# Kernel optimization log

Hardware: AMD Instinct MI355X
Metric: run time of the kernel (lower is better)

The kernel has to match this reference:

```python
import jax, jax.numpy as jnp
import numpy as np

DIM = 768
NUM_HEADS = 12
HEAD_DIM = DIM // NUM_HEADS
SCALE = HEAD_DIM ** -0.5
B, N = 8, 1024


def setup_inputs() -> dict:
    key = jax.random.key(0)
    k1, k2, k3, k4 = jax.random.split(key, 4)
    s = 1.0 / np.sqrt(DIM)
    return {
        "x": jax.random.normal(k1, (B, N, DIM), dtype=jnp.float32),
        "w_qkv": jax.random.normal(k2, (DIM, 3 * DIM), dtype=jnp.float32) * s,  # qkv_bias=False
        "w_proj": jax.random.normal(k3, (DIM, DIM), dtype=jnp.float32) * s,
        "b_proj": jax.random.normal(k4, (DIM,), dtype=jnp.float32) * 0.01,
    }


def reference(x, w_qkv, w_proj, b_proj):
    Bb, Nn, C = x.shape
    qkv = x @ w_qkv  # [B, N, 3C]
    qkv = qkv.reshape(Bb, Nn, 3, NUM_HEADS, HEAD_DIM)
    q = qkv[:, :, 0].transpose(0, 2, 1, 3)  # [B, H, N, d]
    k = qkv[:, :, 1].transpose(0, 2, 1, 3)
    v = qkv[:, :, 2].transpose(0, 2, 1, 3)
    attn = jnp.einsum("bhqd,bhkd->bhqk", q, k) * SCALE
    attn = jax.nn.softmax(attn, axis=-1)  # dropout p=0 -> identity
    out = jnp.einsum("bhqk,bhkd->bhqd", attn, v)
    out = out.transpose(0, 2, 1, 3).reshape(Bb, Nn, C)
    return out @ w_proj + b_proj
```

## Files before the change

### kernel.cpp

```cpp
#include <hip/hip_runtime.h>
#include <stdint.h>

typedef __attribute__((ext_vector_type(8))) __bf16 bf16x8;
typedef __attribute__((ext_vector_type(8))) unsigned short u16x8;
typedef __attribute__((ext_vector_type(4))) unsigned short u16x4;
typedef __attribute__((ext_vector_type(4))) short s16x4;
typedef __attribute__((ext_vector_type(4))) float f32x4;

typedef unsigned int u32_as1 __attribute__((address_space(1)));
typedef unsigned int u32_as3 __attribute__((address_space(3)));

__device__ __forceinline__ unsigned short f2bf(float f) {
  unsigned int u = __float_as_uint(f);
  u += 0x7fffu + ((u >> 16) & 1u);
  return (unsigned short)(u >> 16);
}

__device__ __forceinline__ bf16x8 ld_frag(const unsigned short* p) {
  return __builtin_bit_cast(bf16x8, *(const u16x8*)p);
}

__device__ __forceinline__ f32x4 mfma16(s16x4 a, s16x4 b, f32x4 c) {
#if __has_builtin(__builtin_amdgcn_mfma_f32_16x16x16bf16_1k)
  return __builtin_amdgcn_mfma_f32_16x16x16bf16_1k(a, b, c, 0, 0, 0);
#elif __has_builtin(__builtin_amdgcn_mfma_f32_16x16x16_bf16_1k)
  return __builtin_amdgcn_mfma_f32_16x16x16_bf16_1k(a, b, c, 0, 0, 0);
#else
  asm volatile("v_mfma_f32_16x16x16_bf16 %0, %1, %2, %0"
               : "+v"(c) : "v"(a), "v"(b));
  return c;
#endif
}

__device__ __forceinline__ float fast_exp2(float x) {
#if __has_builtin(__builtin_amdgcn_exp2f)
  return __builtin_amdgcn_exp2f(x);
#else
  return exp2f(x);
#endif
}

__device__ __forceinline__ void async16(const void* g, void* l) {
  const u32_as1* gp = (const u32_as1*)(uintptr_t)g;
  u32_as3* lp = (u32_as3*)(uintptr_t)l;
  __builtin_amdgcn_global_load_lds(gp, lp, 16, 0, 0);
}

template <int N> __device__ __forceinline__ void wait_vmcnt() {
  if constexpr (N == 0) asm volatile("s_waitcnt vmcnt(0)" ::: "memory");
  else if constexpr (N == 3) asm volatile("s_waitcnt vmcnt(3)" ::: "memory");
  else if constexpr (N == 4) asm volatile("s_waitcnt vmcnt(4)" ::: "memory");
}
__device__ __forceinline__ void barrier_raw() {
  asm volatile("s_barrier" ::: "memory");
}

__global__ __launch_bounds__(256) void prep_kernel(
    const float* __restrict__ x, const float* __restrict__ w_qkv,
    const float* __restrict__ w_proj, u16x4* __restrict__ x_bf,
    unsigned short* __restrict__ wqkvT, unsigned short* __restrict__ wprojT) {
  const int bid = blockIdx.x;
  const int t = threadIdx.x;
  if (bid < 6144) {
    const int i = bid * 256 + t;
    float4 v = ((const float4*)x)[i];
    u16x4 o;
    o[0] = f2bf(v.x); o[1] = f2bf(v.y); o[2] = f2bf(v.z); o[3] = f2bf(v.w);
    x_bf[i] = o;
    return;
  }
  __shared__ float tile[32][33];
  const float* w; unsigned short* wt; int N, bx, by;
  if (bid < 6144 + 1728) { const int r = bid - 6144; w = w_qkv; wt = wqkvT; N = 2304; bx = r % 72; by = r / 72; }
  else                   { const int r = bid - 7872; w = w_proj; wt = wprojT; N = 768; bx = r % 24; by = r / 24; }
  const int n0 = bx * 32, k0 = by * 32;
  const int tx = t & 31, ty = t >> 5;
#pragma unroll
  for (int r = 0; r < 4; r++)
    tile[ty + r * 8][tx] = w[(k0 + ty + r * 8) * N + n0 + tx];
  __syncthreads();
#pragma unroll
  for (int r = 0; r < 4; r++)
    wt[(n0 + ty + r * 8) * 768 + k0 + tx] = f2bf(tile[tx][ty + r * 8]);
}

template <int EPI, int NT, int NBLK>
__global__ __launch_bounds__(256, 4) void gemm_bt(
    const unsigned short* __restrict__ A, const unsigned short* __restrict__ Bt,
    unsigned short* __restrict__ qb, unsigned short* __restrict__ kb,
    unsigned short* __restrict__ vtb, float* __restrict__ outp,
    const float* __restrict__ bias) {
  constexpr int STAGE = 4096 + NT * 2048;
  constexpr int NK = 24;
  constexpr int NL = NT + 2;
  __shared__ unsigned short smem[3 * STAGE];

  const int t = threadIdx.x;
  const int lane = t & 63, w = t >> 6;
  const int quad = lane >> 4, l15 = lane & 15;

  const int bid = blockIdx.x;
  const int xcd = bid & 7, slot = bid >> 3;
  const int m0 = (xcd * 8 + slot / NBLK) * 128;
  const int n0 = (slot % NBLK) * (NT * 64);
  const int wm = (w & 1) * 64, wn = (w >> 1) * (NT * 32);

  f32x4 acc[4][NT * 2];
  const f32x4 fzero = {0.f, 0.f, 0.f, 0.f};
#pragma unroll
  for (int i = 0; i < 4; i++)
#pragma unroll
    for (int j = 0; j < NT * 2; j++) acc[i][j] = fzero;

  const int srow = w * 16 + (lane >> 2);
  const int scol = (((lane & 3) - (srow >> 1)) & 3) * 8;
  const unsigned short* Ag = A + (m0 + srow) * 768 + scol;
  const unsigned short* Bg = Bt + (n0 + srow) * 768 + scol;
  const int ldso = w * 512 + lane * 8;

  auto fill = [&](int ktile, int buf) {
    const int kcol = ktile * 32;
    unsigned short* As = smem + buf * STAGE;
    unsigned short* Bs = As + 4096;
    async16(Ag + kcol, As + ldso);
    async16(Ag + 64 * 768 + kcol, As + ldso + 2048);
#pragma unroll
    for (int f = 0; f < NT; f++)
      async16(Bg + f * 64 * 768 + kcol, Bs + ldso + f * 2048);
  };

  fill(0, 0);
  fill(1, 1);
  int cur = 0;
  for (int k = 0; k < NK; ++k) {
    if (k < NK - 1) wait_vmcnt<NL>(); else wait_vmcnt<0>();
    barrier_raw();
    if (k + 2 < NK) {
      int tgt = cur + 2; if (tgt >= 3) tgt -= 3;
      fill(k + 2, tgt);
    }
    const unsigned short* As = smem + cur * STAGE;
    const unsigned short* Bs = As + 4096;

    bf16x8 af[4], bfr[NT * 2];
#pragma unroll
    for (int i = 0; i < 4; i++) {
      const int row = wm + i * 16 + l15;
      af[i] = ld_frag(As + row * 32 + (((quad + (row >> 1)) & 3) << 3));
    }
#pragma unroll
    for (int j = 0; j < NT * 2; j++) {
      const int row = wn + j * 16 + l15;
      bfr[j] = ld_frag(Bs + row * 32 + (((quad + (row >> 1)) & 3) << 3));
    }
#pragma unroll
    for (int i = 0; i < 4; i++)
#pragma unroll
      for (int j = 0; j < NT * 2; j++)
        acc[i][j] = __builtin_amdgcn_mfma_f32_16x16x32_bf16(af[i], bfr[j], acc[i][j], 0, 0, 0);

    cur += 1; if (cur == 3) cur = 0;
  }

#pragma unroll
  for (int i = 0; i < 4; i++) {
    const int gmb = m0 + wm + i * 16 + quad * 4;
#pragma unroll
    for (int j = 0; j < NT * 2; j++) {
      const int gc = n0 + wn + j * 16 + l15;
#pragma unroll
      for (int r = 0; r < 4; r++) {
        const int gm = gmb + r;
        float v = acc[i][j][r];
        if (EPI == 0) {
          const int b = gm >> 10, tok = gm & 1023;
          const int which = (gc >= 1536) ? 2 : (gc >= 768 ? 1 : 0);
          const int rem = gc - which * 768;
          const int h = rem >> 6, d = rem & 63;
          const int bh = b * 12 + h;
          const unsigned short bv = f2bf(v);
          if (which == 0)      qb[(bh << 16) + (tok << 6) + d] = bv;
          else if (which == 1) kb[(bh << 16) + (tok << 6) + d] = bv;
          else                 vtb[(bh << 16) + (d << 10) + tok] = bv;
        } else {
          outp[gm * 768 + gc] = v + bias[gc];
        }
      }
    }
  }
}

#define SWZC(row, c) (((row) << 6) + ((((c) + (row)) & 7) << 3))
#define C2 0.1803368801111244f

__global__ __launch_bounds__(256, 3) void attn_kernel(
    const unsigned short* __restrict__ qb, const unsigned short* __restrict__ kb,
    const unsigned short* __restrict__ vtb, unsigned short* __restrict__ aout) {
  __shared__ unsigned short smem[3 * 8192];

  const int t = threadIdx.x;
  const int lane = t & 63, w = t >> 6;
  const int quad = lane >> 4, l15 = lane & 15;
  const int bh = blockIdx.x;
  const int b = bh / 12, h = bh - b * 12;
  const int q0 = blockIdx.y * 128;
  const int base = bh << 16;

  bf16x8 qf[2][2];
#pragma unroll
  for (int qt = 0; qt < 2; qt++)
#pragma unroll
    for (int s = 0; s < 2; s++)
      qf[qt][s] = ld_frag(qb + base + ((q0 + w * 32 + qt * 16 + l15) << 6) +
                          s * 32 + quad * 8);

  f32x4 oacc[4][2];
  const f32x4 fzero = {0.f, 0.f, 0.f, 0.f};
#pragma unroll
  for (int dt = 0; dt < 4; dt++) { oacc[dt][0] = fzero; oacc[dt][1] = fzero; }
  float lsum0 = 0.f, lsum1 = 0.f;

  const int srow = t >> 3, schk = t & 7;
  const int c0 = ((schk - srow) & 7) * 8;
  const int c1 = ((schk - (srow + 32)) & 7) * 8;

  auto fillkv = [&](int tile, int buf) {
    const int kv0 = tile * 64;
    unsigned short* Ks = smem + buf * 8192;
    unsigned short* Vts = Ks + 4096;
    async16(kb + base + ((kv0 + srow) << 6) + c0, Ks + t * 8);
    async16(kb + base + ((kv0 + srow + 32) << 6) + c1, Ks + 2048 + t * 8);
    async16(vtb + base + (srow << 10) + kv0 + c0, Vts + t * 8);
    async16(vtb + base + ((srow + 32) << 10) + kv0 + c1, Vts + 2048 + t * 8);
  };

  fillkv(0, 0);
  fillkv(1, 1);
  int cur = 0;
  for (int it = 0; it < 16; ++it) {
    if (it < 15) wait_vmcnt<4>(); else wait_vmcnt<0>();
    barrier_raw();
    if (it + 2 < 16) {
      int tgt = cur + 2; if (tgt >= 3) tgt -= 3;
      fillkv(it + 2, tgt);
    }
    const unsigned short* Ks = smem + cur * 8192;
    const unsigned short* Vts = Ks + 4096;

    f32x4 st[4][2];
#pragma unroll
    for (int tc = 0; tc < 4; tc++) { st[tc][0] = fzero; st[tc][1] = fzero; }
#pragma unroll
    for (int s = 0; s < 2; s++) {
#pragma unroll
      for (int tc = 0; tc < 4; tc++) {
        const bf16x8 kf = ld_frag(Ks + SWZC(tc * 16 + l15, s * 4 + quad));
        st[tc][0] = __builtin_amdgcn_mfma_f32_16x16x32_bf16(kf, qf[0][s], st[tc][0], 0, 0, 0);
        st[tc][1] = __builtin_amdgcn_mfma_f32_16x16x32_bf16(kf, qf[1][s], st[tc][1], 0, 0, 0);
      }
    }

    s16x4 pf[4][2];
#pragma unroll
    for (int tc = 0; tc < 4; tc++) {
#pragma unroll
      for (int qt = 0; qt < 2; qt++) {
        const float p0 = fast_exp2(st[tc][qt][0] * C2);
        const float p1 = fast_exp2(st[tc][qt][1] * C2);
        const float p2 = fast_exp2(st[tc][qt][2] * C2);
        const float p3 = fast_exp2(st[tc][qt][3] * C2);
        const float ps = (p0 + p1) + (p2 + p3);
        if (qt == 0) lsum0 += ps; else lsum1 += ps;
        s16x4 pk;
        pk[0] = (short)f2bf(p0); pk[1] = (short)f2bf(p1);
        pk[2] = (short)f2bf(p2); pk[3] = (short)f2bf(p3);
        pf[tc][qt] = pk;
      }
    }

#pragma unroll
    for (int tc = 0; tc < 4; tc++) {
#pragma unroll
      for (int dt = 0; dt < 4; dt++) {
        const int row = dt * 16 + l15;
        const int addr = (row << 6) + ((((tc * 2 + (quad >> 1)) + row) & 7) << 3) +
                         ((quad & 1) << 2);
        const s16x4 vf = *(const s16x4*)(Vts + addr);
        oacc[dt][0] = mfma16(vf, pf[tc][0], oacc[dt][0]);
        oacc[dt][1] = mfma16(vf, pf[tc][1], oacc[dt][1]);
      }
    }

    cur += 1; if (cur == 3) cur = 0;
  }

  lsum0 += __shfl_xor(lsum0, 16); lsum0 += __shfl_xor(lsum0, 32);
  lsum1 += __shfl_xor(lsum1, 16); lsum1 += __shfl_xor(lsum1, 32);
  const float inv0 = 1.f / lsum0, inv1 = 1.f / lsum1;

  __syncthreads();
  unsigned short* Ot = smem;
#pragma unroll
  for (int dt = 0; dt < 4; dt++) {
#pragma unroll
    for (int qt = 0; qt < 2; qt++) {
      const float inv = qt == 0 ? inv0 : inv1;
      const int qrow = (w * 32 + qt * 16 + l15) * 72 + dt * 16 + quad * 4;
#pragma unroll
      for (int r = 0; r < 4; r++)
        Ot[qrow + r] = f2bf(oacc[dt][qt][r] * inv);
    }
  }
  __syncthreads();
#pragma unroll
  for (int it = 0; it < 4; it++) {
    const int q = it * 32 + (t >> 3);
    const int d0 = (t & 7) * 8;
    const u16x8 v = *(const u16x8*)(Ot + q * 72 + d0);
    *(u16x8*)(aout + (b * 1024 + q0 + q) * 768 + h * 64 + d0) = v;
  }
}

extern "C" void kernel_launch(void* const* d_in, const int* in_sizes, int n_in,
                              void* d_out, int out_size, void* d_ws, size_t ws_size,
                              hipStream_t stream) {
  (void)in_sizes; (void)n_in; (void)out_size; (void)ws_size;
  const float* x = (const float*)d_in[0];
  const float* w_qkv = (const float*)d_in[1];
  const float* w_proj = (const float*)d_in[2];
  const float* b_proj = (const float*)d_in[3];
  float* out = (float*)d_out;

  char* ws = (char*)d_ws;
  unsigned short* x_bf   = (unsigned short*)(ws);
  unsigned short* wqkvT  = (unsigned short*)(ws + 12582912);
  unsigned short* wprojT = (unsigned short*)(ws + 16121856);
  unsigned short* qb     = (unsigned short*)(ws + 17301504);
  unsigned short* kb     = (unsigned short*)(ws + 29884416);
  unsigned short* vtb    = (unsigned short*)(ws + 42467328);
  unsigned short* aout   = x_bf;

  prep_kernel<<<8448, 256, 0, stream>>>(x, w_qkv, w_proj, (u16x4*)x_bf, wqkvT, wprojT);
  gemm_bt<0, 2, 18><<<1152, 256, 0, stream>>>(x_bf, wqkvT, qb, kb, vtb, nullptr, nullptr);
  attn_kernel<<<dim3(96, 8), 256, 0, stream>>>(qb, kb, vtb, aout);
  gemm_bt<1, 1, 12><<<768, 256, 0, stream>>>(aout, wprojT, nullptr, nullptr, nullptr, out, b_proj);
}
```

Before: 202.4 us.

## Replace async global-to-LDS triple buffering with register-staged double buffering in GEMM

The GEMM kernels stop using direct global_load_lds into a three-stage LDS ring. They now load tiles into registers two steps ahead and write them to a two-stage LDS buffer after each compute step, with an lgkmcnt wait plus barrier. Minimum waves per EU for the QKV GEMM drops from 4 to 3, which leaves room for the extra staging registers. This cuts LDS footprint and changes the load/compute overlap, at the cost of more VGPR pressure, possibly lower occupancy, and extra ds_write instructions.

New measurement: 199.6 us. About the same (-1.4%).

```diff
diff --git a/kernel.cpp b/kernel.cpp
--- a/kernel.cpp
+++ b/kernel.cpp
@@ -46,13 +46,12 @@
   __builtin_amdgcn_global_load_lds(gp, lp, 16, 0, 0);
 }
 
+__device__ __forceinline__ void lds_barrier() {
+  asm volatile("s_waitcnt lgkmcnt(0)\ns_barrier" ::: "memory");
+}
 template <int N> __device__ __forceinline__ void wait_vmcnt() {
   if constexpr (N == 0) asm volatile("s_waitcnt vmcnt(0)" ::: "memory");
-  else if constexpr (N == 3) asm volatile("s_waitcnt vmcnt(3)" ::: "memory");
   else if constexpr (N == 4) asm volatile("s_waitcnt vmcnt(4)" ::: "memory");
-}
-__device__ __forceinline__ void barrier_raw() {
-  asm volatile("s_barrier" ::: "memory");
 }
 
 __global__ __launch_bounds__(256) void prep_kernel(
@@ -84,16 +83,16 @@
     wt[(n0 + ty + r * 8) * 768 + k0 + tx] = f2bf(tile[tx][ty + r * 8]);
 }
 
-template <int EPI, int NT, int NBLK>
-__global__ __launch_bounds__(256, 4) void gemm_bt(
+template <int EPI, int NT, int NBLK, int MINW>
+__global__ __launch_bounds__(256, MINW) void gemm_bt(
     const unsigned short* __restrict__ A, const unsigned short* __restrict__ Bt,
     unsigned short* __restrict__ qb, unsigned short* __restrict__ kb,
     unsigned short* __restrict__ vtb, float* __restrict__ outp,
     const float* __restrict__ bias) {
   constexpr int STAGE = 4096 + NT * 2048;
   constexpr int NK = 24;
-  constexpr int NL = NT + 2;
-  __shared__ unsigned short smem[3 * STAGE];
+  constexpr int NLD = 2 + NT;
+  __shared__ unsigned short smem[2 * STAGE];
 
   const int t = threadIdx.x;
   const int lane = t & 63, w = t >> 6;
@@ -118,28 +117,33 @@
   const unsigned short* Bg = Bt + (n0 + srow) * 768 + scol;
   const int ldso = w * 512 + lane * 8;
 
-  auto fill = [&](int ktile, int buf) {
-    const int kcol = ktile * 32;
-    unsigned short* As = smem + buf * STAGE;
-    unsigned short* Bs = As + 4096;
-    async16(Ag + kcol, As + ldso);
-    async16(Ag + 64 * 768 + kcol, As + ldso + 2048);
+  u16x8 rb[2][NLD];
+
+  auto g2r = [&](int k, u16x8* r) {
+    r[0] = *(const u16x8*)(Ag + k * 32);
+    r[1] = *(const u16x8*)(Ag + 64 * 768 + k * 32);
 #pragma unroll
     for (int f = 0; f < NT; f++)
-      async16(Bg + f * 64 * 768 + kcol, Bs + ldso + f * 2048);
+      r[2 + f] = *(const u16x8*)(Bg + f * 64 * 768 + k * 32);
   };
-
-  fill(0, 0);
-  fill(1, 1);
-  int cur = 0;
+  auto r2l = [&](int k, const u16x8* r) {
+    unsigned short* As = smem + (k & 1) * STAGE;
+    *(u16x8*)(As + ldso) = r[0];
+    *(u16x8*)(As + ldso + 2048) = r[1];
+#pragma unroll
+    for (int f = 0; f < NT; f++)
+      *(u16x8*)(As + 4096 + ldso + f * 2048) = r[2 + f];
+  };
+
+  g2r(0, rb[0]);
+  g2r(1, rb[1]);
+  r2l(0, rb[0]);
+  lds_barrier();
+  g2r(2, rb[0]);
+
+#pragma unroll
   for (int k = 0; k < NK; ++k) {
-    if (k < NK - 1) wait_vmcnt<NL>(); else wait_vmcnt<0>();
-    barrier_raw();
-    if (k + 2 < NK) {
-      int tgt = cur + 2; if (tgt >= 3) tgt -= 3;
-      fill(k + 2, tgt);
-    }
-    const unsigned short* As = smem + cur * STAGE;
+    const unsigned short* As = smem + (k & 1) * STAGE;
     const unsigned short* Bs = As + 4096;
 
     bf16x8 af[4], bfr[NT * 2];
@@ -159,7 +163,9 @@
       for (int j = 0; j < NT * 2; j++)
         acc[i][j] = __builtin_amdgcn_mfma_f32_16x16x32_bf16(af[i], bfr[j], acc[i][j], 0, 0, 0);
 
-    cur += 1; if (cur == 3) cur = 0;
+    if (k + 1 < NK) r2l(k + 1, rb[(k + 1) & 1]);
+    if (k + 3 < NK) g2r(k + 3, rb[(k + 1) & 1]);
+    if (k + 1 < NK) lds_barrier();
   }
 
 #pragma unroll
@@ -239,7 +245,7 @@
   int cur = 0;
   for (int it = 0; it < 16; ++it) {
     if (it < 15) wait_vmcnt<4>(); else wait_vmcnt<0>();
-    barrier_raw();
+    asm volatile("s_barrier" ::: "memory");
     if (it + 2 < 16) {
       int tgt = cur + 2; if (tgt >= 3) tgt -= 3;
       fillkv(it + 2, tgt);
@@ -341,7 +347,7 @@
   unsigned short* aout   = x_bf;
 
   prep_kernel<<<8448, 256, 0, stream>>>(x, w_qkv, w_proj, (u16x4*)x_bf, wqkvT, wprojT);
-  gemm_bt<0, 2, 18><<<1152, 256, 0, stream>>>(x_bf, wqkvT, qb, kb, vtb, nullptr, nullptr);
+  gemm_bt<0, 2, 18, 3><<<1152, 256, 0, stream>>>(x_bf, wqkvT, qb, kb, vtb, nullptr, nullptr);
   attn_kernel<<<dim3(96, 8), 256, 0, stream>>>(qb, kb, vtb, aout);
-  gemm_bt<1, 1, 12><<<768, 256, 0, stream>>>(aout, wprojT, nullptr, nullptr, nullptr, out, b_proj);
-}
+  gemm_bt<1, 1, 12, 4><<<768, 256, 0, stream>>>(aout, wprojT, nullptr, nullptr, nullptr, out, b_proj);
+}
```

## Replace LDS-staged GEMM with direct global-to-register double-buffered loads

Applied to the files above, without the earlier changes.

The QKV and projection GEMMs no longer stage A and B tiles through LDS with async global_load_lds and a three-buffer ring plus barriers. Each wave now loads its MFMA fragments straight from global memory into registers, double-buffered one k-step ahead with the loop fully unrolled. Launch-bounds occupancy hints are lowered to 2 and 3 waves per SIMD. This removes the LDS round trip and block-wide barriers, but gives up reuse of shared tiles between waves, so global and L2 traffic rises and register pressure grows.

New measurement: 320.7 us. 1.58x slower.

```diff
diff --git a/kernel.cpp b/kernel.cpp
--- a/kernel.cpp
+++ b/kernel.cpp
@@ -18,6 +18,9 @@
 
 __device__ __forceinline__ bf16x8 ld_frag(const unsigned short* p) {
   return __builtin_bit_cast(bf16x8, *(const u16x8*)p);
+}
+__device__ __forceinline__ bf16x8 as_bf(u16x8 v) {
+  return __builtin_bit_cast(bf16x8, v);
 }
 
 __device__ __forceinline__ f32x4 mfma16(s16x4 a, s16x4 b, f32x4 c) {
@@ -48,11 +51,7 @@
 
 template <int N> __device__ __forceinline__ void wait_vmcnt() {
   if constexpr (N == 0) asm volatile("s_waitcnt vmcnt(0)" ::: "memory");
-  else if constexpr (N == 3) asm volatile("s_waitcnt vmcnt(3)" ::: "memory");
   else if constexpr (N == 4) asm volatile("s_waitcnt vmcnt(4)" ::: "memory");
-}
-__device__ __forceinline__ void barrier_raw() {
-  asm volatile("s_barrier" ::: "memory");
 }
 
 __global__ __launch_bounds__(256) void prep_kernel(
@@ -84,17 +83,13 @@
     wt[(n0 + ty + r * 8) * 768 + k0 + tx] = f2bf(tile[tx][ty + r * 8]);
 }
 
-template <int EPI, int NT, int NBLK>
-__global__ __launch_bounds__(256, 4) void gemm_bt(
+template <int EPI, int NT, int NBLK, int MINW>
+__global__ __launch_bounds__(256, MINW) void gemm_direct(
     const unsigned short* __restrict__ A, const unsigned short* __restrict__ Bt,
     unsigned short* __restrict__ qb, unsigned short* __restrict__ kb,
     unsigned short* __restrict__ vtb, float* __restrict__ outp,
     const float* __restrict__ bias) {
-  constexpr int STAGE = 4096 + NT * 2048;
   constexpr int NK = 24;
-  constexpr int NL = NT + 2;
-  __shared__ unsigned short smem[3 * STAGE];
-
   const int t = threadIdx.x;
   const int lane = t & 63, w = t >> 6;
   const int quad = lane >> 4, l15 = lane & 15;
@@ -105,6 +100,9 @@
   const int n0 = (slot % NBLK) * (NT * 64);
   const int wm = (w & 1) * 64, wn = (w >> 1) * (NT * 32);
 
+  const unsigned short* Ap = A + (m0 + wm + l15) * 768 + quad * 8;
+  const unsigned short* Bp = Bt + (n0 + wn + l15) * 768 + quad * 8;
+
   f32x4 acc[4][NT * 2];
   const f32x4 fzero = {0.f, 0.f, 0.f, 0.f};
 #pragma unroll
@@ -112,54 +110,27 @@
 #pragma unroll
     for (int j = 0; j < NT * 2; j++) acc[i][j] = fzero;
 
-  const int srow = w * 16 + (lane >> 2);
-  const int scol = (((lane & 3) - (srow >> 1)) & 3) * 8;
-  const unsigned short* Ag = A + (m0 + srow) * 768 + scol;
-  const unsigned short* Bg = Bt + (n0 + srow) * 768 + scol;
-  const int ldso = w * 512 + lane * 8;
-
-  auto fill = [&](int ktile, int buf) {
-    const int kcol = ktile * 32;
-    unsigned short* As = smem + buf * STAGE;
-    unsigned short* Bs = As + 4096;
-    async16(Ag + kcol, As + ldso);
-    async16(Ag + 64 * 768 + kcol, As + ldso + 2048);
-#pragma unroll
-    for (int f = 0; f < NT; f++)
-      async16(Bg + f * 64 * 768 + kcol, Bs + ldso + f * 2048);
+  u16x8 ar[2][4], br[2][NT * 2];
+  auto g2r = [&](int k, int s) {
+#pragma unroll
+    for (int i = 0; i < 4; i++)
+      ar[s][i] = *(const u16x8*)(Ap + i * 16 * 768 + k * 32);
+#pragma unroll
+    for (int j = 0; j < NT * 2; j++)
+      br[s][j] = *(const u16x8*)(Bp + j * 16 * 768 + k * 32);
   };
 
-  fill(0, 0);
-  fill(1, 1);
-  int cur = 0;
+  g2r(0, 0);
+#pragma unroll
   for (int k = 0; k < NK; ++k) {
-    if (k < NK - 1) wait_vmcnt<NL>(); else wait_vmcnt<0>();
-    barrier_raw();
-    if (k + 2 < NK) {
-      int tgt = cur + 2; if (tgt >= 3) tgt -= 3;
-      fill(k + 2, tgt);
-    }
-    const unsigned short* As = smem + cur * STAGE;
-    const unsigned short* Bs = As + 4096;
-
-    bf16x8 af[4], bfr[NT * 2];
-#pragma unroll
-    for (int i = 0; i < 4; i++) {
-      const int row = wm + i * 16 + l15;
-      af[i] = ld_frag(As + row * 32 + (((quad + (row >> 1)) & 3) << 3));
-    }
-#pragma unroll
-    for (int j = 0; j < NT * 2; j++) {
-      const int row = wn + j * 16 + l15;
-      bfr[j] = ld_frag(Bs + row * 32 + (((quad + (row >> 1)) & 3) << 3));
-    }
+    if (k + 1 < NK) g2r(k + 1, (k + 1) & 1);
+    const int s = k & 1;
 #pragma unroll
     for (int i = 0; i < 4; i++)
 #pragma unroll
       for (int j = 0; j < NT * 2; j++)
-        acc[i][j] = __builtin_amdgcn_mfma_f32_16x16x32_bf16(af[i], bfr[j], acc[i][j], 0, 0, 0);
-
-    cur += 1; if (cur == 3) cur = 0;
+        acc[i][j] = __builtin_amdgcn_mfma_f32_16x16x32_bf16(
+            as_bf(ar[s][i]), as_bf(br[s][j]), acc[i][j], 0, 0, 0);
   }
 
 #pragma unroll
@@ -239,7 +210,7 @@
   int cur = 0;
   for (int it = 0; it < 16; ++it) {
     if (it < 15) wait_vmcnt<4>(); else wait_vmcnt<0>();
-    barrier_raw();
+    asm volatile("s_barrier" ::: "memory");
     if (it + 2 < 16) {
       int tgt = cur + 2; if (tgt >= 3) tgt -= 3;
       fillkv(it + 2, tgt);
@@ -341,7 +312,7 @@
   unsigned short* aout   = x_bf;
 
   prep_kernel<<<8448, 256, 0, stream>>>(x, w_qkv, w_proj, (u16x4*)x_bf, wqkvT, wprojT);
-  gemm_bt<0, 2, 18><<<1152, 256, 0, stream>>>(x_bf, wqkvT, qb, kb, vtb, nullptr, nullptr);
+  gemm_direct<0, 2, 18, 2><<<1152, 256, 0, stream>>>(x_bf, wqkvT, qb, kb, vtb, nullptr, nullptr);
   attn_kernel<<<dim3(96, 8), 256, 0, stream>>>(qb, kb, vtb, aout);
-  gemm_bt<1, 1, 12><<<768, 256, 0, stream>>>(aout, wprojT, nullptr, nullptr, nullptr, out, b_proj);
-}
+  gemm_direct<1, 1, 12, 3><<<768, 256, 0, stream>>>(aout, wprojT, nullptr, nullptr, nullptr, out, b_proj);
+}
```
